# Kernel tuning notes

Measured on AMD Instinct MI355X. Metric: run time of the kernel, lower is better.

Reference implementation:

```python
import jax, jax.numpy as jnp
import numpy as np

N = 50000   # nodes
E = 800000  # edges (avg degree 16)
F_IN = 128
H = 128
L = 4
LN_EPS = 1e-5


def setup_inputs() -> dict:
    key = jax.random.key(0)
    ks = jax.random.split(key, 4)
    x = jax.random.normal(ks[0], (N, F_IN), dtype=jnp.float32)
    edge_index = jax.random.randint(ks[1], (2, E), 0, N)
    conv_w = jax.random.normal(ks[2], (L, F_IN, H), dtype=jnp.float32) * 0.05
    conv_b = jnp.zeros((L, H), dtype=jnp.float32)
    ln_g = jnp.ones((L, H), dtype=jnp.float32)
    ln_b = jnp.zeros((L, H), dtype=jnp.float32)
    head_w = jax.random.normal(ks[3], (H, 1), dtype=jnp.float32) * 0.05
    head_b = jnp.zeros((1,), dtype=jnp.float32)
    return {"x": x, "edge_index": edge_index, "conv_w": conv_w, "conv_b": conv_b,
            "ln_g": ln_g, "ln_b": ln_b, "head_w": head_w, "head_b": head_b}


def _layer_norm(h, g, b):
    mu = jnp.mean(h, axis=-1, keepdims=True)
    var = jnp.mean(jnp.square(h - mu), axis=-1, keepdims=True)
    return (h - mu) * jax.lax.rsqrt(var + LN_EPS) * g + b


def _gcn_conv(h, W, b, src, dst, inv_sqrt_deg, inv_deg):
    # PyG GCNConv: self-loops + symmetric normalization D^-1/2 (A+I) D^-1/2, then bias.
    hw = h @ W  # (N, H)
    norm = inv_sqrt_deg[src] * inv_sqrt_deg[dst]  # (E,)
    msg = hw[src] * norm[:, None]  # gather + edgewise scale
    agg = jax.ops.segment_sum(msg, dst, num_segments=N)  # scatter-add
    agg = agg + hw * inv_deg[:, None]  # self-loop term (norm = 1/deg)
    return agg + b


def reference(x, edge_index, conv_w, conv_b, ln_g, ln_b, head_w, head_b):
    src, dst = edge_index[0], edge_index[1]
    # degree on target nodes, including self-loop
    deg = jax.ops.segment_sum(jnp.ones((E,), x.dtype), dst, num_segments=N) + 1.0
    inv_sqrt_deg = jax.lax.rsqrt(deg)
    inv_deg = 1.0 / deg
    h = x
    for i in range(L):
        h = _gcn_conv(h, conv_w[i], conv_b[i], src, dst, inv_sqrt_deg, inv_deg)
        h = _layer_norm(h, ln_g[i], ln_b[i])
        if i != L - 1:
            h = jax.nn.gelu(h, approximate=False)
            # dropout is identity in eval mode
    scores = (h @ head_w + head_b).squeeze(-1)  # (N,)
    return scores, h
```

## Files before the change

kernel.cpp:

```cpp
#include <hip/hip_runtime.h>
#include <math.h>

#define N_NODES 50000
#define N_EDGES 800000
#define HDIM 128
#define NLAYERS 4
#define LN_EPS 1e-5f
#define EQUARTER (N_EDGES / 4)
#define SEG 64
#define FILLB ((EQUARTER + 255) / 256)
#define GEMMB ((N_NODES + 63) / 64)

typedef __attribute__((ext_vector_type(8))) short short8;
typedef __attribute__((ext_vector_type(4))) float floatx4;

__device__ __forceinline__ ushort f2bf(float x) {
    unsigned b = __float_as_uint(x);
    unsigned r = b + 0x7fffu + ((b >> 16) & 1u);
    return (ushort)(r >> 16);
}
__device__ __forceinline__ float2 bf2f2(unsigned u) {
    return make_float2(__uint_as_float(u << 16), __uint_as_float(u & 0xffff0000u));
}


__device__ __forceinline__ void fill_body(int bid, int tid, const int* __restrict__ src,
                                          const int* __restrict__ dst, int* __restrict__ cnt,
                                          ushort* __restrict__ csr16) {
    int t = bid * 256 + tid;
    if (t >= EQUARTER) return;
    int s0 = src[t],                d0 = dst[t];
    int s1 = src[t + EQUARTER],     d1 = dst[t + EQUARTER];
    int s2 = src[t + 2 * EQUARTER], d2 = dst[t + 2 * EQUARTER];
    int s3 = src[t + 3 * EQUARTER], d3 = dst[t + 3 * EQUARTER];
    int p0 = atomicAdd(&cnt[d0], 1);
    int p1 = atomicAdd(&cnt[d1], 1);
    int p2 = atomicAdd(&cnt[d2], 1);
    int p3 = atomicAdd(&cnt[d3], 1);
    if (p0 < SEG) csr16[d0 * SEG + p0] = (ushort)s0;
    if (p1 < SEG) csr16[d1 * SEG + p1] = (ushort)s1;
    if (p2 < SEG) csr16[d2 * SEG + p2] = (ushort)s2;
    if (p3 < SEG) csr16[d3 * SEG + p3] = (ushort)s3;
}

__global__ __launch_bounds__(256) void isd_kernel(const int* __restrict__ cnt,
                                                  float* __restrict__ isd,
                                                  float* __restrict__ ind) {
    int i = blockIdx.x * 256 + threadIdx.x;
    if (i < N_NODES) {
        float d = (float)cnt[i] + 1.0f;
        isd[i] = rsqrtf(d);
        ind[i] = 1.0f / d;
    }
}

__global__ __launch_bounds__(256) void bprep_kernel(const float* __restrict__ W,
                                                    ushort* __restrict__ bfrag) {
    int idx = blockIdx.x * 256 + threadIdx.x;
    if (idx >= NLAYERS * 4 * 8 * 64) return;
    int lane = idx & 63;
    int t = (idx >> 6) & 7;
    int s = (idx >> 9) & 3;
    int l = idx >> 11;
    int n = t * 16 + (lane & 15);
    int kb = s * 32 + (lane >> 4) * 8;
    const float* Wl = W + (size_t)l * HDIM * HDIM;
    union { uint4 q; ushort u[8]; } o;
#pragma unroll
    for (int j = 0; j < 8; ++j) o.u[j] = f2bf(Wl[(size_t)(kb + j) * HDIM + n]);
    *(uint4*)&bfrag[(size_t)idx * 8] = o.q;
}

template <bool A_FP32>
__device__ __forceinline__ void gemm_body(int bid, int tid, const void* __restrict__ Av,
                                          const ushort* __restrict__ bfrag,
                                          ushort* __restrict__ out) {
    int wave = tid >> 6, lane = tid & 63;
    int quad = lane >> 4, mrow = lane & 15;
    int rowBase = bid * 64 + wave * 16;
    int arow = rowBase + mrow;
    bool aok = arow < N_NODES;

    floatx4 acc[8];
#pragma unroll
    for (int t = 0; t < 8; ++t) acc[t] = (floatx4)0.f;

#pragma unroll
    for (int s = 0; s < 4; ++s) {
        union { short8 v; ushort u[8]; } af;
        if (A_FP32) {
            const float* A = (const float*)Av;
            if (aok) {
                const float* p = &A[(size_t)arow * HDIM + s * 32 + quad * 8];
#pragma unroll
                for (int j = 0; j < 8; ++j) af.u[j] = f2bf(p[j]);
            } else {
#pragma unroll
                for (int j = 0; j < 8; ++j) af.u[j] = 0;
            }
        } else {
            const ushort* A = (const ushort*)Av;
            if (aok) {
                af.v = *(const short8*)&A[(size_t)arow * HDIM + s * 32 + quad * 8];
            } else {
#pragma unroll
                for (int j = 0; j < 8; ++j) af.u[j] = 0;
            }
        }
#pragma unroll
        for (int t = 0; t < 8; ++t) {
            short8 bf = *(const short8*)&bfrag[(size_t)(((s * 8 + t) * 64) + lane) * 8];
            acc[t] = __builtin_amdgcn_mfma_f32_16x16x32_bf16(af.v, bf, acc[t], 0, 0, 0);
        }
    }
#pragma unroll
    for (int t = 0; t < 8; ++t) {
#pragma unroll
        for (int r = 0; r < 4; ++r) {
            int row = rowBase + quad * 4 + r;
            if (row < N_NODES) out[(size_t)row * HDIM + t * 16 + mrow] = f2bf(acc[t][r]);
        }
    }
}

__global__ __launch_bounds__(256) void fused0_kernel(
    const int* __restrict__ src, const int* __restrict__ dst, int* __restrict__ cnt,
    ushort* __restrict__ csr16, const float* __restrict__ x,
    const ushort* __restrict__ bfrag0, ushort* __restrict__ hw) {
    if (blockIdx.x < FILLB)
        fill_body(blockIdx.x, threadIdx.x, src, dst, cnt, csr16);
    else
        gemm_body<true>(blockIdx.x - FILLB, threadIdx.x, x, bfrag0, hw);
}

__global__ __launch_bounds__(256) void gemm_mfma_kernel(const ushort* __restrict__ A,
                                                        const ushort* __restrict__ bfrag,
                                                        ushort* __restrict__ out) {
    gemm_body<false>(blockIdx.x, threadIdx.x, A, bfrag, out);
}

__global__ __launch_bounds__(256) void agg_ln_kernel(
    const uint2* __restrict__ hw2, const int* __restrict__ degcnt,
    const ushort* __restrict__ csr16, const float* __restrict__ isd,
    const float* __restrict__ ind, const float* __restrict__ conv_b,
    const float* __restrict__ ln_g, const float* __restrict__ ln_b,
    uint2* __restrict__ hout_bf, float* __restrict__ hout_f32,
    const float* __restrict__ head_w, const float* __restrict__ head_b,
    float* __restrict__ scores, int final_layer) {
    int wave = threadIdx.x >> 6;
    int lane = threadIdx.x & 63;
    int g = lane >> 5;
    int li = lane & 31;
    int n = blockIdx.x * 4 + wave;
    if (n >= N_NODES) return;
    int c = li * 4;

    float isd_n = isd[n], ind_n = ind[n];
    int rs = n * SEG;
    int deg = min(degcnt[n], SEG);

    float e0 = 0.f, e1 = 0.f, e2 = 0.f, e3 = 0.f;
    int sj = 0;
    float wj = 0.f;
    if (lane < deg) {
        sj = (int)csr16[rs + lane];
        wj = isd[sj];
    }
    for (int j = 0; j < deg; j += 8) {
#pragma unroll
        for (int t = 0; t < 4; ++t) {
            int idx = j + 2 * t + g;
            int s = __shfl(sj, idx);
            float w = __shfl(wj, idx);
            uint2 u = hw2[(size_t)s * 32 + li];
            float2 q0 = bf2f2(u.x), q1 = bf2f2(u.y);
            e0 = fmaf(q0.x, w, e0); e1 = fmaf(q0.y, w, e1);
            e2 = fmaf(q1.x, w, e2); e3 = fmaf(q1.y, w, e3);
        }
    }
    e0 += __shfl_xor(e0, 32); e1 += __shfl_xor(e1, 32);
    e2 += __shfl_xor(e2, 32); e3 += __shfl_xor(e3, 32);

    uint2 hv = hw2[(size_t)n * 32 + li];
    float2 h0 = bf2f2(hv.x), h1 = bf2f2(hv.y);
    float4 cb = *(const float4*)&conv_b[c];
    float a0 = fmaf(e0, isd_n, fmaf(h0.x, ind_n, cb.x));
    float a1 = fmaf(e1, isd_n, fmaf(h0.y, ind_n, cb.y));
    float a2 = fmaf(e2, isd_n, fmaf(h1.x, ind_n, cb.z));
    float a3 = fmaf(e3, isd_n, fmaf(h1.y, ind_n, cb.w));

    float sum = a0 + a1 + a2 + a3;
#pragma unroll
    for (int o = 1; o < 32; o <<= 1) sum += __shfl_xor(sum, o);
    float mu = sum * (1.0f / HDIM);
    float d0 = a0 - mu, d1 = a1 - mu, d2 = a2 - mu, d3 = a3 - mu;
    float vs = d0 * d0 + d1 * d1 + d2 * d2 + d3 * d3;
#pragma unroll
    for (int o = 1; o < 32; o <<= 1) vs += __shfl_xor(vs, o);
    float rstd = rsqrtf(vs * (1.0f / HDIM) + LN_EPS);
    float4 gv = *(const float4*)&ln_g[c];
    float4 bv = *(const float4*)&ln_b[c];
    float y0 = fmaf(d0 * rstd, gv.x, bv.x);
    float y1 = fmaf(d1 * rstd, gv.y, bv.y);
    float y2 = fmaf(d2 * rstd, gv.z, bv.z);
    float y3 = fmaf(d3 * rstd, gv.w, bv.w);

    if (!final_layer) {
#define GELU(v) ((v) = 0.5f * (v) * (1.0f + erff((v) * 0.70710678118654752f)))
        GELU(y0); GELU(y1); GELU(y2); GELU(y3);
#undef GELU
        if (g == 0) {
            uint2 ov;
            ov.x = (unsigned)f2bf(y0) | ((unsigned)f2bf(y1) << 16);
            ov.y = (unsigned)f2bf(y2) | ((unsigned)f2bf(y3) << 16);
            hout_bf[(size_t)n * 32 + li] = ov;
        }
    } else {
        if (g == 0)
            *(float4*)&hout_f32[(size_t)n * HDIM + c] = make_float4(y0, y1, y2, y3);
        float4 hwv = *(const float4*)&head_w[c];
        float p = y0 * hwv.x + y1 * hwv.y + y2 * hwv.z + y3 * hwv.w;
#pragma unroll
        for (int o = 1; o < 32; o <<= 1) p += __shfl_xor(p, o);
        if (lane == 0) scores[n] = p + head_b[0];
    }
}


extern "C" void kernel_launch(void* const* d_in, const int* in_sizes, int n_in,
                              void* d_out, int out_size, void* d_ws, size_t ws_size,
                              hipStream_t stream) {
    const float* x      = (const float*)d_in[0];
    const int*   eidx   = (const int*)d_in[1];
    const float* conv_w = (const float*)d_in[2];
    const float* conv_b = (const float*)d_in[3];
    const float* ln_g   = (const float*)d_in[4];
    const float* ln_b   = (const float*)d_in[5];
    const float* head_w = (const float*)d_in[6];
    const float* head_b = (const float*)d_in[7];
    float* out = (float*)d_out;

    const int* src = eidx;
    const int* dst = eidx + N_EDGES;

    char* ws = (char*)d_ws;
    size_t o = 0;
    auto alloc = [&](size_t elems) {
        void* p = ws + o * 4;
        o += (elems + 15) & ~(size_t)15;
        return p;
    };
    int*      cnt      = (int*)alloc(N_NODES);
    float*    isd      = (float*)alloc(N_NODES);
    float*    ind      = (float*)alloc(N_NODES);
    ushort*   csr16    = (ushort*)alloc((size_t)N_NODES * SEG / 2);
    ushort*   bfrag    = (ushort*)alloc(NLAYERS * 4 * 8 * 64 * 8 / 2);
    unsigned* hw       = (unsigned*)alloc((size_t)N_NODES * 64);
    unsigned* hbuf     = (unsigned*)alloc((size_t)N_NODES * 64);

    hipMemsetAsync(cnt, 0, N_NODES * sizeof(int), stream);
    bprep_kernel<<<(NLAYERS * 4 * 8 * 64 + 255) / 256, 256, 0, stream>>>(conv_w, bfrag);
    fused0_kernel<<<FILLB + GEMMB, 256, 0, stream>>>(src, dst, cnt, csr16, x, bfrag,
                                                     (ushort*)hw);
    isd_kernel<<<(N_NODES + 255) / 256, 256, 0, stream>>>(cnt, isd, ind);

    const unsigned* hin = hw;
    for (int l = 0; l < NLAYERS; ++l) {
        if (l > 0) {
            const ushort* bl = bfrag + (size_t)l * 4 * 8 * 64 * 8;
            gemm_mfma_kernel<<<GEMMB, 256, 0, stream>>>((const ushort*)hbuf, bl, (ushort*)hw);
        }
        int fin = (l == NLAYERS - 1) ? 1 : 0;
        agg_ln_kernel<<<(N_NODES + 3) / 4, 256, 0, stream>>>(
            (const uint2*)hw, cnt, csr16, isd, ind,
            conv_b + (size_t)l * HDIM, ln_g + (size_t)l * HDIM, ln_b + (size_t)l * HDIM,
            (uint2*)hbuf, out + N_NODES, head_w, head_b, out, fin);
    }
}
```

Baseline: 349.8 us.

## Widen aggregation gathers to 16-byte loads and fold degree-norm kernels inline

Removes the memset and the separate inverse-degree kernel: cnt is zeroed inside the weight-prep kernel, and the normalisation factors are recomputed from cnt inside the aggregation kernel. The aggregation now maps 16 lanes per feature row with 128-bit loads, processing four neighbors per wave step instead of two. This cuts launch overhead and gather instruction count, at the cost of extra rsqrt work and more registers per thread.

After: 370.4 us. 1.06x slower.

```diff
diff --git a/kernel.cpp b/kernel.cpp
--- a/kernel.cpp
+++ b/kernel.cpp
@@ -10,6 +10,7 @@
 #define SEG 64
 #define FILLB ((EQUARTER + 255) / 256)
 #define GEMMB ((N_NODES + 63) / 64)
+#define BPREPB 64
 
 typedef __attribute__((ext_vector_type(8))) short short8;
 typedef __attribute__((ext_vector_type(4))) float floatx4;
@@ -43,20 +44,11 @@
     if (p3 < SEG) csr16[d3 * SEG + p3] = (ushort)s3;
 }
 
-__global__ __launch_bounds__(256) void isd_kernel(const int* __restrict__ cnt,
-                                                  float* __restrict__ isd,
-                                                  float* __restrict__ ind) {
-    int i = blockIdx.x * 256 + threadIdx.x;
-    if (i < N_NODES) {
-        float d = (float)cnt[i] + 1.0f;
-        isd[i] = rsqrtf(d);
-        ind[i] = 1.0f / d;
-    }
-}
-
 __global__ __launch_bounds__(256) void bprep_kernel(const float* __restrict__ W,
-                                                    ushort* __restrict__ bfrag) {
+                                                    ushort* __restrict__ bfrag,
+                                                    int* __restrict__ cnt) {
     int idx = blockIdx.x * 256 + threadIdx.x;
+    for (int i = idx; i < N_NODES; i += BPREPB * 256) cnt[i] = 0;
     if (idx >= NLAYERS * 4 * 8 * 64) return;
     int lane = idx & 63;
     int t = (idx >> 6) & 7;
@@ -140,88 +132,113 @@
 }
 
 __global__ __launch_bounds__(256) void agg_ln_kernel(
-    const uint2* __restrict__ hw2, const int* __restrict__ degcnt,
-    const ushort* __restrict__ csr16, const float* __restrict__ isd,
-    const float* __restrict__ ind, const float* __restrict__ conv_b,
+    const uint4* __restrict__ hw4, const int* __restrict__ cnt,
+    const ushort* __restrict__ csr16, const float* __restrict__ conv_b,
     const float* __restrict__ ln_g, const float* __restrict__ ln_b,
-    uint2* __restrict__ hout_bf, float* __restrict__ hout_f32,
+    uint4* __restrict__ hout_bf, float* __restrict__ hout_f32,
     const float* __restrict__ head_w, const float* __restrict__ head_b,
     float* __restrict__ scores, int final_layer) {
     int wave = threadIdx.x >> 6;
     int lane = threadIdx.x & 63;
-    int g = lane >> 5;
-    int li = lane & 31;
+    int g = lane >> 4;
+    int li = lane & 15;
     int n = blockIdx.x * 4 + wave;
     if (n >= N_NODES) return;
-    int c = li * 4;
-
-    float isd_n = isd[n], ind_n = ind[n];
+    int c = li * 8;
+
+    int true_deg = cnt[n];
+    float dnf = (float)true_deg + 1.0f;
+    float isd_n = rsqrtf(dnf);
+    float ind_n = 1.0f / dnf;
     int rs = n * SEG;
-    int deg = min(degcnt[n], SEG);
-
-    float e0 = 0.f, e1 = 0.f, e2 = 0.f, e3 = 0.f;
+    int deg = min(true_deg, SEG);
+
+    float e0 = 0.f, e1 = 0.f, e2 = 0.f, e3 = 0.f, e4 = 0.f, e5 = 0.f, e6 = 0.f, e7 = 0.f;
     int sj = 0;
     float wj = 0.f;
     if (lane < deg) {
         sj = (int)csr16[rs + lane];
-        wj = isd[sj];
-    }
-    for (int j = 0; j < deg; j += 8) {
+        wj = rsqrtf((float)cnt[sj] + 1.0f);
+    }
+    for (int j = 0; j < deg; j += 16) {
 #pragma unroll
         for (int t = 0; t < 4; ++t) {
-            int idx = j + 2 * t + g;
+            int idx = j + 4 * t + g;
             int s = __shfl(sj, idx);
             float w = __shfl(wj, idx);
-            uint2 u = hw2[(size_t)s * 32 + li];
+            uint4 u = hw4[(size_t)s * 16 + li];
             float2 q0 = bf2f2(u.x), q1 = bf2f2(u.y);
+            float2 q2 = bf2f2(u.z), q3 = bf2f2(u.w);
             e0 = fmaf(q0.x, w, e0); e1 = fmaf(q0.y, w, e1);
             e2 = fmaf(q1.x, w, e2); e3 = fmaf(q1.y, w, e3);
-        }
-    }
-    e0 += __shfl_xor(e0, 32); e1 += __shfl_xor(e1, 32);
-    e2 += __shfl_xor(e2, 32); e3 += __shfl_xor(e3, 32);
-
-    uint2 hv = hw2[(size_t)n * 32 + li];
-    float2 h0 = bf2f2(hv.x), h1 = bf2f2(hv.y);
-    float4 cb = *(const float4*)&conv_b[c];
-    float a0 = fmaf(e0, isd_n, fmaf(h0.x, ind_n, cb.x));
-    float a1 = fmaf(e1, isd_n, fmaf(h0.y, ind_n, cb.y));
-    float a2 = fmaf(e2, isd_n, fmaf(h1.x, ind_n, cb.z));
-    float a3 = fmaf(e3, isd_n, fmaf(h1.y, ind_n, cb.w));
-
-    float sum = a0 + a1 + a2 + a3;
-#pragma unroll
-    for (int o = 1; o < 32; o <<= 1) sum += __shfl_xor(sum, o);
+            e4 = fmaf(q2.x, w, e4); e5 = fmaf(q2.y, w, e5);
+            e6 = fmaf(q3.x, w, e6); e7 = fmaf(q3.y, w, e7);
+        }
+    }
+#define XG(E) E += __shfl_xor(E, 16); E += __shfl_xor(E, 32);
+    XG(e0) XG(e1) XG(e2) XG(e3) XG(e4) XG(e5) XG(e6) XG(e7)
+#undef XG
+
+    uint4 hv = hw4[(size_t)n * 16 + li];
+    float2 h0 = bf2f2(hv.x), h1 = bf2f2(hv.y), h2 = bf2f2(hv.z), h3 = bf2f2(hv.w);
+    float4 cb0 = *(const float4*)&conv_b[c];
+    float4 cb1 = *(const float4*)&conv_b[c + 4];
+    float a0 = fmaf(e0, isd_n, fmaf(h0.x, ind_n, cb0.x));
+    float a1 = fmaf(e1, isd_n, fmaf(h0.y, ind_n, cb0.y));
+    float a2 = fmaf(e2, isd_n, fmaf(h1.x, ind_n, cb0.z));
+    float a3 = fmaf(e3, isd_n, fmaf(h1.y, ind_n, cb0.w));
+    float a4 = fmaf(e4, isd_n, fmaf(h2.x, ind_n, cb1.x));
+    float a5 = fmaf(e5, isd_n, fmaf(h2.y, ind_n, cb1.y));
+    float a6 = fmaf(e6, isd_n, fmaf(h3.x, ind_n, cb1.z));
+    float a7 = fmaf(e7, isd_n, fmaf(h3.y, ind_n, cb1.w));
+
+    float sum = a0 + a1 + a2 + a3 + a4 + a5 + a6 + a7;
+#pragma unroll
+    for (int o = 1; o < 16; o <<= 1) sum += __shfl_xor(sum, o);
     float mu = sum * (1.0f / HDIM);
     float d0 = a0 - mu, d1 = a1 - mu, d2 = a2 - mu, d3 = a3 - mu;
-    float vs = d0 * d0 + d1 * d1 + d2 * d2 + d3 * d3;
-#pragma unroll
-    for (int o = 1; o < 32; o <<= 1) vs += __shfl_xor(vs, o);
+    float d4 = a4 - mu, d5 = a5 - mu, d6 = a6 - mu, d7 = a7 - mu;
+    float vs = d0 * d0 + d1 * d1 + d2 * d2 + d3 * d3 + d4 * d4 + d5 * d5 + d6 * d6 + d7 * d7;
+#pragma unroll
+    for (int o = 1; o < 16; o <<= 1) vs += __shfl_xor(vs, o);
     float rstd = rsqrtf(vs * (1.0f / HDIM) + LN_EPS);
-    float4 gv = *(const float4*)&ln_g[c];
-    float4 bv = *(const float4*)&ln_b[c];
-    float y0 = fmaf(d0 * rstd, gv.x, bv.x);
-    float y1 = fmaf(d1 * rstd, gv.y, bv.y);
-    float y2 = fmaf(d2 * rstd, gv.z, bv.z);
-    float y3 = fmaf(d3 * rstd, gv.w, bv.w);
+    float4 g0 = *(const float4*)&ln_g[c];
+    float4 g1 = *(const float4*)&ln_g[c + 4];
+    float4 b0 = *(const float4*)&ln_b[c];
+    float4 b1 = *(const float4*)&ln_b[c + 4];
+    float y0 = fmaf(d0 * rstd, g0.x, b0.x);
+    float y1 = fmaf(d1 * rstd, g0.y, b0.y);
+    float y2 = fmaf(d2 * rstd, g0.z, b0.z);
+    float y3 = fmaf(d3 * rstd, g0.w, b0.w);
+    float y4 = fmaf(d4 * rstd, g1.x, b1.x);
+    float y5 = fmaf(d5 * rstd, g1.y, b1.y);
+    float y6 = fmaf(d6 * rstd, g1.z, b1.z);
+    float y7 = fmaf(d7 * rstd, g1.w, b1.w);
 
     if (!final_layer) {
 #define GELU(v) ((v) = 0.5f * (v) * (1.0f + erff((v) * 0.70710678118654752f)))
         GELU(y0); GELU(y1); GELU(y2); GELU(y3);
+        GELU(y4); GELU(y5); GELU(y6); GELU(y7);
 #undef GELU
         if (g == 0) {
-            uint2 ov;
+            uint4 ov;
             ov.x = (unsigned)f2bf(y0) | ((unsigned)f2bf(y1) << 16);
             ov.y = (unsigned)f2bf(y2) | ((unsigned)f2bf(y3) << 16);
-            hout_bf[(size_t)n * 32 + li] = ov;
+            ov.z = (unsigned)f2bf(y4) | ((unsigned)f2bf(y5) << 16);
+            ov.w = (unsigned)f2bf(y6) | ((unsigned)f2bf(y7) << 16);
+            hout_bf[(size_t)n * 16 + li] = ov;
         }
     } else {
-        if (g == 0)
+        if (g == 0) {
             *(float4*)&hout_f32[(size_t)n * HDIM + c] = make_float4(y0, y1, y2, y3);
-        float4 hwv = *(const float4*)&head_w[c];
-        float p = y0 * hwv.x + y1 * hwv.y + y2 * hwv.z + y3 * hwv.w;
-#pragma unroll
-        for (int o = 1; o < 32; o <<= 1) p += __shfl_xor(p, o);
+            *(float4*)&hout_f32[(size_t)n * HDIM + c + 4] = make_float4(y4, y5, y6, y7);
+        }
+        float4 hw0 = *(const float4*)&head_w[c];
+        float4 hw1 = *(const float4*)&head_w[c + 4];
+        float p = y0 * hw0.x + y1 * hw0.y + y2 * hw0.z + y3 * hw0.w +
+                  y4 * hw1.x + y5 * hw1.y + y6 * hw1.z + y7 * hw1.w;
+#pragma unroll
+        for (int o = 1; o < 16; o <<= 1) p += __shfl_xor(p, o);
         if (lane == 0) scores[n] = p + head_b[0];
     }
 }
@@ -251,20 +268,15 @@
         return p;
     };
     int*      cnt      = (int*)alloc(N_NODES);
-    float*    isd      = (float*)alloc(N_NODES);
-    float*    ind      = (float*)alloc(N_NODES);
     ushort*   csr16    = (ushort*)alloc((size_t)N_NODES * SEG / 2);
     ushort*   bfrag    = (ushort*)alloc(NLAYERS * 4 * 8 * 64 * 8 / 2);
     unsigned* hw       = (unsigned*)alloc((size_t)N_NODES * 64);
     unsigned* hbuf     = (unsigned*)alloc((size_t)N_NODES * 64);
 
-    hipMemsetAsync(cnt, 0, N_NODES * sizeof(int), stream);
-    bprep_kernel<<<(NLAYERS * 4 * 8 * 64 + 255) / 256, 256, 0, stream>>>(conv_w, bfrag);
+    bprep_kernel<<<BPREPB, 256, 0, stream>>>(conv_w, bfrag, cnt);
     fused0_kernel<<<FILLB + GEMMB, 256, 0, stream>>>(src, dst, cnt, csr16, x, bfrag,
                                                      (ushort*)hw);
-    isd_kernel<<<(N_NODES + 255) / 256, 256, 0, stream>>>(cnt, isd, ind);
-
-    const unsigned* hin = hw;
+
     for (int l = 0; l < NLAYERS; ++l) {
         if (l > 0) {
             const ushort* bl = bfrag + (size_t)l * 4 * 8 * 64 * 8;
@@ -272,8 +284,8 @@
         }
         int fin = (l == NLAYERS - 1) ? 1 : 0;
         agg_ln_kernel<<<(N_NODES + 3) / 4, 256, 0, stream>>>(
-            (const uint2*)hw, cnt, csr16, isd, ind,
+            (const uint4*)hw, cnt, csr16,
             conv_b + (size_t)l * HDIM, ln_g + (size_t)l * HDIM, ln_b + (size_t)l * HDIM,
-            (uint2*)hbuf, out + N_NODES, head_w, head_b, out, fin);
-    }
-}
+            (uint4*)hbuf, out + N_NODES, head_w, head_b, out, fin);
+    }
+}
```
